# Performance work log

Measured on AMD Instinct MI355X. Metric: run time of the kernel, lower is better.

The kernel has to match this reference:

```python
import jax, jax.numpy as jnp
import numpy as np

N, E, D_IN, HID, D_OUT = 200000, 5000000, 128, 16, 2


def setup_inputs() -> dict:
    key = jax.random.key(0)
    ks = jax.random.split(key, 8)
    x = jax.random.normal(ks[0], (N, D_IN), dtype=jnp.float32)
    edge_index = jax.random.randint(ks[1], (2, E), 0, N, dtype=jnp.int32)
    W1 = jax.random.normal(ks[2], (D_IN, HID), dtype=jnp.float32) / np.sqrt(D_IN)
    b1 = jnp.zeros((HID,), dtype=jnp.float32)
    W3 = jax.random.normal(ks[3], (HID, HID), dtype=jnp.float32) / np.sqrt(HID)
    b3 = jnp.zeros((HID,), dtype=jnp.float32)
    W2 = jax.random.normal(ks[4], (HID, D_OUT), dtype=jnp.float32) / np.sqrt(HID)
    b2 = jnp.zeros((D_OUT,), dtype=jnp.float32)
    return {"x": x, "edge_index": edge_index, "W1": W1, "b1": b1,
            "W3": W3, "b3": b3, "W2": W2, "b2": b2}


def reference(x, edge_index, W1, b1, W3, b3, W2, b2):
    # GCNConv: add self-loops, symmetric normalization, aggregate, linear+bias.
    src, dst = edge_index[0], edge_index[1]
    loops = jnp.arange(N, dtype=src.dtype)
    src_f = jnp.concatenate([src, loops])  # [E+N]
    dst_f = jnp.concatenate([dst, loops])
    deg = jax.ops.segment_sum(jnp.ones_like(src_f, dtype=jnp.float32), dst_f,
                              num_segments=N)
    dis = jnp.where(deg > 0, jax.lax.rsqrt(jnp.maximum(deg, 1.0)), 0.0)
    norm = dis[src_f] * dis[dst_f]  # [E+N]

    def gcn_conv(h, W, b):
        h = h @ W                                   # [N, F_out] small GEMM
        msg = h[src_f] * norm[:, None]              # gather + scale
        agg = jax.ops.segment_sum(msg, dst_f, num_segments=N)  # scatter-add
        return agg + b

    h = jax.nn.relu(gcn_conv(x, W1, b1))    # conv1 (dropout is identity in eval)
    h = jax.nn.relu(gcn_conv(h, W3, b3))    # conv3 loop (conv_number-2 = 1 iter)
    h = gcn_conv(h, W2, b2)                 # conv2
    return jax.nn.log_softmax(h, axis=1)
```

## Files before the change

### kernel.cpp

```cpp
#include <hip/hip_runtime.h>

#define NN 200000
#define NE 5000000
#define DIN 128
#define HID 16
#define DOUT 2
#define BSZ 391
#define NB 512
#define LBITS 9
#define NCH 4
#define SLICE_DIV 50000
#define NK (NB * NCH)
#define NKB 512
#define SKEYS 2048
#define PB 512
#define PT 512
#define ECAP 9216

static_assert((size_t)NB * BSZ >= NN, "bucket coverage");
static_assert((NN - 1) / SLICE_DIV == NCH - 1, "slice count");
static_assert(NE % 8 == 0, "int4-pair edge reads");


__global__ __launch_bounds__(PT) void hist_pass(const int4* __restrict__ dst4,
                                                int* __restrict__ blockHist) {
    __shared__ int h[NKB];
    for (int k = threadIdx.x; k < NKB; k += PT) h[k] = 0;
    __syncthreads();
    const int NI8 = NE / 8;
    for (int j = blockIdx.x * PT + threadIdx.x; j < NI8; j += PB * PT) {
        int4 d0 = dst4[2 * j];
        int4 d1 = dst4[2 * j + 1];
        atomicAdd(&h[d0.x / BSZ], 1);
        atomicAdd(&h[d0.y / BSZ], 1);
        atomicAdd(&h[d0.z / BSZ], 1);
        atomicAdd(&h[d0.w / BSZ], 1);
        atomicAdd(&h[d1.x / BSZ], 1);
        atomicAdd(&h[d1.y / BSZ], 1);
        atomicAdd(&h[d1.z / BSZ], 1);
        atomicAdd(&h[d1.w / BSZ], 1);
    }
    __syncthreads();
    for (int k = threadIdx.x; k < NKB; k += PT)
        blockHist[(size_t)blockIdx.x * NKB + k] = h[k];
}

__global__ __launch_bounds__(256) void tot_pass(const int* __restrict__ blockHist,
                                                int* __restrict__ chunkStart) {
    int k = blockIdx.x * 256 + threadIdx.x;
    if (k >= NKB) return;
    int s = 0;
#pragma unroll 16
    for (int b = 0; b < PB; ++b) s += blockHist[(size_t)b * NKB + k];
    chunkStart[k] = s;
}

__global__ __launch_bounds__(NKB) void scan_keys(int* __restrict__ chunkStart) {
    __shared__ int wsum[8];
    int t = threadIdx.x;
    int lane = t & 63, w = t >> 6;
    int v = chunkStart[t];
    int inc = v;
    for (int off = 1; off < 64; off <<= 1) {
        int nb = __shfl_up(inc, off, 64);
        if (lane >= off) inc += nb;
    }
    if (lane == 63) wsum[w] = inc;
    __syncthreads();
    if (t == 0) {
        int car = 0;
#pragma unroll
        for (int i = 0; i < 8; ++i) { int u = wsum[i]; wsum[i] = car; car += u; }
    }
    __syncthreads();
    chunkStart[t] = inc - v + wsum[w];
    if (t == 0) chunkStart[NKB] = NE;
}

__global__ __launch_bounds__(256) void offsets_pass(int* __restrict__ blockHist,
                                                    const int* __restrict__ chunkStart) {
    int k = blockIdx.x * 256 + threadIdx.x;
    if (k >= NKB) return;
    int r = chunkStart[k];
#pragma unroll 8
    for (int b = 0; b < PB; ++b) {
        size_t idx = (size_t)b * NKB + k;
        int v = blockHist[idx];
        blockHist[idx] = r;
        r += v;
    }
}

__global__ __launch_bounds__(PT) void scatter_pass(const int4* __restrict__ src4,
                                                   const int4* __restrict__ dst4,
                                                   const int* __restrict__ blockHist,
                                                   unsigned* __restrict__ pedge) {
    __shared__ int cur[NKB];
    for (int k = threadIdx.x; k < NKB; k += PT)
        cur[k] = blockHist[(size_t)blockIdx.x * NKB + k];
    __syncthreads();
    const int NI8 = NE / 8;
    for (int j = blockIdx.x * PT + threadIdx.x; j < NI8; j += PB * PT) {
        int4 s0 = src4[2 * j];
        int4 s1 = src4[2 * j + 1];
        int4 d0 = dst4[2 * j];
        int4 d1 = dst4[2 * j + 1];
        int b0 = d0.x / BSZ, b1 = d0.y / BSZ, b2 = d0.z / BSZ, b3 = d0.w / BSZ;
        int b4 = d1.x / BSZ, b5 = d1.y / BSZ, b6 = d1.z / BSZ, b7 = d1.w / BSZ;
        int p0 = atomicAdd(&cur[b0], 1);
        int p1 = atomicAdd(&cur[b1], 1);
        int p2 = atomicAdd(&cur[b2], 1);
        int p3 = atomicAdd(&cur[b3], 1);
        int p4 = atomicAdd(&cur[b4], 1);
        int p5 = atomicAdd(&cur[b5], 1);
        int p6 = atomicAdd(&cur[b6], 1);
        int p7 = atomicAdd(&cur[b7], 1);
        pedge[p0] = ((unsigned)s0.x << LBITS) | (unsigned)(d0.x - b0 * BSZ);
        pedge[p1] = ((unsigned)s0.y << LBITS) | (unsigned)(d0.y - b1 * BSZ);
        pedge[p2] = ((unsigned)s0.z << LBITS) | (unsigned)(d0.z - b2 * BSZ);
        pedge[p3] = ((unsigned)s0.w << LBITS) | (unsigned)(d0.w - b3 * BSZ);
        pedge[p4] = ((unsigned)s1.x << LBITS) | (unsigned)(d1.x - b4 * BSZ);
        pedge[p5] = ((unsigned)s1.y << LBITS) | (unsigned)(d1.y - b5 * BSZ);
        pedge[p6] = ((unsigned)s1.z << LBITS) | (unsigned)(d1.z - b6 * BSZ);
        pedge[p7] = ((unsigned)s1.w << LBITS) | (unsigned)(d1.w - b7 * BSZ);
    }
}


__global__ __launch_bounds__(512) void subsort(const unsigned* __restrict__ pedge,
                                               const int* __restrict__ chunkStart,
                                               int* __restrict__ pedge2,
                                               int* __restrict__ rowStart,
                                               float* __restrict__ dis) {
    __shared__ int h[SKEYS];
    __shared__ unsigned ebuf[ECAP];
    __shared__ int wsum[8];
    int t = threadIdx.x;
    int b = blockIdx.x;
    int lane = t & 63, w = t >> 6;
    int e0 = chunkStart[b], e1 = chunkStart[b + 1];
    int n = e1 - e0;
    for (int k = t; k < SKEYS; k += 512) h[k] = 0;
    __syncthreads();
    for (int i = t; i < n; i += 512) {
        unsigned p = pedge[e0 + i];
        if (i < ECAP) ebuf[i] = p;
        int sv = (int)(p >> LBITS);
        atomicAdd(&h[(sv / SLICE_DIV) * 512 + (p & 511u)], 1);
    }
    __syncthreads();
    if (t < BSZ) {
        int dg = 1;
#pragma unroll
        for (int s = 0; s < NCH; ++s) dg += h[s * 512 + t];
        int node = b * BSZ + t;
        if (node < NN) dis[node] = rsqrtf((float)dg);
    }
    int vals[4];
    int s = 0;
#pragma unroll
    for (int j = 0; j < 4; ++j) { vals[j] = h[t * 4 + j]; s += vals[j]; }
    int inc = s;
    for (int off = 1; off < 64; off <<= 1) {
        int nb = __shfl_up(inc, off, 64);
        if (lane >= off) inc += nb;
    }
    if (lane == 63) wsum[w] = inc;
    __syncthreads();
    if (t == 0) {
        int car = 0;
#pragma unroll
        for (int i = 0; i < 8; ++i) { int u = wsum[i]; wsum[i] = car; car += u; }
    }
    __syncthreads();
    int run = inc - s + wsum[w];
#pragma unroll
    for (int j = 0; j < 4; ++j) {
        int k = t * 4 + j;
        h[k] = run;
        int dl = k & 511, sl = k >> 9;
        if (dl < BSZ)
            rowStart[(size_t)(b * NCH + sl) * BSZ + dl] = e0 + run;
        run += vals[j];
    }
    __syncthreads();
    for (int i = t; i < n; i += 512) {
        unsigned p = (i < ECAP) ? ebuf[i] : pedge[e0 + i];
        int sv = (int)(p >> LBITS);
        int key = (sv / SLICE_DIV) * 512 + (p & 511u);
        int pos = atomicAdd(&h[key], 1);
        pedge2[e0 + pos] = sv;
    }
    if (b == 0 && t == 0) rowStart[(size_t)NK * BSZ] = NE;
}


#define GXT 512
#define GXR 128
__global__ __launch_bounds__(GXT) void gemm_x_w1(const float* __restrict__ x,
                                                 const float* __restrict__ W,
                                                 const float* __restrict__ dis,
                                                 float* __restrict__ out) {
    __shared__ float w[DIN * HID];
    int t = threadIdx.x;
    for (int i = t; i < DIN * HID; i += GXT) w[i] = W[i];
    __syncthreads();
    int row = blockIdx.x * GXR + (t >> 2);
    int c0 = (t & 3) * 4;
    if (row >= NN) return;
    const float4* xr = reinterpret_cast<const float4*>(x + (size_t)row * DIN);
    float ax = 0.f, ay = 0.f, az = 0.f, aw = 0.f;
#pragma unroll
    for (int k4 = 0; k4 < DIN / 4; ++k4) {
        float4 xv = xr[k4];
        float4 w0 = *reinterpret_cast<const float4*>(&w[(4 * k4 + 0) * HID + c0]);
        float4 w1 = *reinterpret_cast<const float4*>(&w[(4 * k4 + 1) * HID + c0]);
        float4 w2 = *reinterpret_cast<const float4*>(&w[(4 * k4 + 2) * HID + c0]);
        float4 w3 = *reinterpret_cast<const float4*>(&w[(4 * k4 + 3) * HID + c0]);
        ax += xv.x * w0.x + xv.y * w1.x + xv.z * w2.x + xv.w * w3.x;
        ay += xv.x * w0.y + xv.y * w1.y + xv.z * w2.y + xv.w * w3.y;
        az += xv.x * w0.z + xv.y * w1.z + xv.z * w2.z + xv.w * w3.z;
        aw += xv.x * w0.w + xv.y * w1.w + xv.z * w2.w + xv.w * w3.w;
    }
    float dd = dis[row];
    *reinterpret_cast<float4*>(&out[(size_t)row * HID + c0]) =
        make_float4(ax * dd, ay * dd, az * dd, aw * dd);
}

__global__ __launch_bounds__(256) void gemm_h_w16(const float* __restrict__ h,
                                                  const float* __restrict__ W,
                                                  const float* __restrict__ dis,
                                                  float* __restrict__ out) {
    __shared__ float w[HID * HID];
    if (threadIdx.x < HID * HID) w[threadIdx.x] = W[threadIdx.x];
    __syncthreads();
    int row = blockIdx.x * 16 + (threadIdx.x >> 4);
    int c = threadIdx.x & 15;
    if (row >= NN) return;
    const float4* hr = reinterpret_cast<const float4*>(h + (size_t)row * HID);
    float acc = 0.f;
#pragma unroll
    for (int k4 = 0; k4 < HID / 4; ++k4) {
        float4 v = hr[k4];
        acc += v.x * w[(4 * k4 + 0) * HID + c] + v.y * w[(4 * k4 + 1) * HID + c]
             + v.z * w[(4 * k4 + 2) * HID + c] + v.w * w[(4 * k4 + 3) * HID + c];
    }
    out[row * HID + c] = acc * dis[row];
}

__global__ __launch_bounds__(256) void gemm_h_w2(const float* __restrict__ h,
                                                 const float* __restrict__ W,
                                                 const float* __restrict__ dis,
                                                 float* __restrict__ out) {
    int t = blockIdx.x * 256 + threadIdx.x;
    int row = t >> 1;
    int c = t & 1;
    if (row >= NN) return;
    const float* hr = h + (size_t)row * HID;
    float acc = 0.f;
#pragma unroll
    for (int k = 0; k < HID; ++k) acc += hr[k] * W[k * DOUT + c];
    out[row * DOUT + c] = acc * dis[row];
}


__device__ __forceinline__ void acc_edges(const int* __restrict__ pedge2,
                                          const float4* __restrict__ xs4,
                                          int e, int e1, int c4, float4& a) {
    for (; e + 3 < e1; e += 4) {
        int s0 = pedge2[e], s1 = pedge2[e + 1];
        int s2 = pedge2[e + 2], s3 = pedge2[e + 3];
        float4 u0 = xs4[(s0 << 2) + c4];
        float4 u1 = xs4[(s1 << 2) + c4];
        float4 u2 = xs4[(s2 << 2) + c4];
        float4 u3 = xs4[(s3 << 2) + c4];
        a.x += (u0.x + u1.x) + (u2.x + u3.x);
        a.y += (u0.y + u1.y) + (u2.y + u3.y);
        a.z += (u0.z + u1.z) + (u2.z + u3.z);
        a.w += (u0.w + u1.w) + (u2.w + u3.w);
    }
    for (; e < e1; ++e) {
        float4 u = xs4[(pedge2[e] << 2) + c4];
        a.x += u.x; a.y += u.y; a.z += u.z; a.w += u.w;
    }
}

__global__ __launch_bounds__(1024, 8) void agg16_all(const int* __restrict__ pedge2,
                                                     const int* __restrict__ rowStart,
                                                     const float* __restrict__ xs,
                                                     const float* __restrict__ dis,
                                                     const float* __restrict__ bias,
                                                     float* __restrict__ buf,
                                                     int relu) {
    int t = threadIdx.x;
    int b = blockIdx.x;
    int base = b * BSZ;
    int c4 = t & 3;
    int q = t >> 2;
    int g0 = (q * BSZ) >> 8;
    int g1 = ((q + 1) * BSZ) >> 8;
    bool two = (g1 - g0) == 2;
    int n0 = base + g0, n1 = base + g0 + 1;
    bool v0 = n0 < NN;
    bool v1 = two && (n1 < NN);
    const float4* xs4 = reinterpret_cast<const float4*>(xs);
    float4* buf4 = reinterpret_cast<float4*>(buf);
    int sA[NCH], sB[NCH], sC[NCH];
#pragma unroll
    for (int r = 0; r < NCH; ++r) {
        const int* rs = rowStart + (size_t)(b * NCH + r) * BSZ + g0;
        sA[r] = v0 ? rs[0] : 0;
        sB[r] = v0 ? rs[1] : 0;
        sC[r] = v1 ? rs[2] : 0;
    }
    float4 a0 = make_float4(0.f, 0.f, 0.f, 0.f);
    float4 a1 = a0;
    if (v0) a0 = xs4[(n0 << 2) + c4];
    if (v1) a1 = xs4[(n1 << 2) + c4];
#pragma unroll
    for (int r = 0; r < NCH; ++r) {
        if (v0) acc_edges(pedge2, xs4, sA[r], sB[r], c4, a0);
        if (v1) acc_edges(pedge2, xs4, sB[r], sC[r], c4, a1);
    }
    float4 bb = reinterpret_cast<const float4*>(bias)[c4];
    if (v0) {
        float dd = dis[n0];
        float4 v = make_float4(dd * a0.x + bb.x, dd * a0.y + bb.y,
                               dd * a0.z + bb.z, dd * a0.w + bb.w);
        if (relu) { v.x = fmaxf(v.x, 0.f); v.y = fmaxf(v.y, 0.f);
                    v.z = fmaxf(v.z, 0.f); v.w = fmaxf(v.w, 0.f); }
        buf4[(n0 << 2) + c4] = v;
    }
    if (v1) {
        float dd = dis[n1];
        float4 v = make_float4(dd * a1.x + bb.x, dd * a1.y + bb.y,
                               dd * a1.z + bb.z, dd * a1.w + bb.w);
        if (relu) { v.x = fmaxf(v.x, 0.f); v.y = fmaxf(v.y, 0.f);
                    v.z = fmaxf(v.z, 0.f); v.w = fmaxf(v.w, 0.f); }
        buf4[(n1 << 2) + c4] = v;
    }
}

__global__ __launch_bounds__(512) void agg2_lsm(const int* __restrict__ pedge2,
                                                const int* __restrict__ rowStart,
                                                const float* __restrict__ xs,
                                                const float* __restrict__ dis,
                                                const float* __restrict__ bias,
                                                float* __restrict__ out) {
    int t = threadIdx.x;
    int b = blockIdx.x;
    if (t >= BSZ) return;
    int node = b * BSZ + t;
    if (node >= NN) return;
    const float2* xs2 = reinterpret_cast<const float2*>(xs);
    float a0 = 0.f, a1 = 0.f;
#pragma unroll
    for (int s = 0; s < NCH; ++s) {
        const int* rs = rowStart + (size_t)(b * NCH + s) * BSZ;
        int e = rs[t], e1 = rs[t + 1];
        for (; e + 3 < e1; e += 4) {
            int s0 = pedge2[e], s1 = pedge2[e + 1];
            int s2 = pedge2[e + 2], s3 = pedge2[e + 3];
            float2 v0 = xs2[s0], v1 = xs2[s1], v2 = xs2[s2], v3 = xs2[s3];
            a0 += (v0.x + v1.x) + (v2.x + v3.x);
            a1 += (v0.y + v1.y) + (v2.y + v3.y);
        }
        for (; e < e1; ++e) {
            float2 v = xs2[pedge2[e]];
            a0 += v.x; a1 += v.y;
        }
    }
    float2 sv = xs2[node];
    float d = dis[node];
    float v0 = (a0 + sv.x) * d + bias[0];
    float v1 = (a1 + sv.y) * d + bias[1];
    float m = fmaxf(v0, v1);
    float lse = m + logf(__expf(v0 - m) + __expf(v1 - m));
    reinterpret_cast<float2*>(out)[node] = make_float2(v0 - lse, v1 - lse);
}


extern "C" void kernel_launch(void* const* d_in, const int* in_sizes, int n_in,
                              void* d_out, int out_size, void* d_ws, size_t ws_size,
                              hipStream_t stream) {
    const float* x = (const float*)d_in[0];
    const int* ei = (const int*)d_in[1];
    const float* W1 = (const float*)d_in[2];
    const float* b1 = (const float*)d_in[3];
    const float* W3 = (const float*)d_in[4];
    const float* b3 = (const float*)d_in[5];
    const float* W2 = (const float*)d_in[6];
    const float* b2 = (const float*)d_in[7];
    float* out = (float*)d_out;

    const int4* src4 = (const int4*)ei;
    const int4* dst4 = (const int4*)(ei + NE);

    int* W = (int*)d_ws;
    unsigned* pedge = (unsigned*)W;
    int* pedge2 = W + NE;
    int* rowStart = W + 2 * (size_t)NE;
    int* blockHist = rowStart + (size_t)NK * BSZ + 4;
    int* chunkStart = blockHist + (size_t)PB * NKB;
    float* dis = (float*)(chunkStart + NKB + 4);
    float* bufB = dis + NN;
    float* bufA = (float*)W;

    const int B = 256;
    auto cdiv = [](long long a, long long b) { return (int)((a + b - 1) / b); };

    hist_pass<<<PB, PT, 0, stream>>>(dst4, blockHist);
    tot_pass<<<cdiv(NKB, 256), 256, 0, stream>>>(blockHist, chunkStart);
    scan_keys<<<1, NKB, 0, stream>>>(chunkStart);
    offsets_pass<<<cdiv(NKB, 256), 256, 0, stream>>>(blockHist, chunkStart);
    scatter_pass<<<PB, PT, 0, stream>>>(src4, dst4, blockHist, pedge);
    subsort<<<NB, 512, 0, stream>>>(pedge, chunkStart, pedge2, rowStart, dis);

    gemm_x_w1<<<cdiv(NN, GXR), GXT, 0, stream>>>(x, W1, dis, bufA);
    agg16_all<<<NB, 1024, 0, stream>>>(pedge2, rowStart, bufA, dis, b1, bufB, 1);

    gemm_h_w16<<<cdiv(NN, 16), B, 0, stream>>>(bufB, W3, dis, bufA);
    agg16_all<<<NB, 1024, 0, stream>>>(pedge2, rowStart, bufA, dis, b3, bufB, 1);

    gemm_h_w2<<<cdiv((long long)NN * DOUT, B), B, 0, stream>>>(bufB, W2, dis, bufA);
    agg2_lsm<<<NB, 512, 0, stream>>>(pedge2, rowStart, bufA, dis, b2, out);
}
```

Before: 276.3 us.

## Fuse next-layer small GEMMs into aggregation epilogues via quad shuffles

Removes the two standalone small-GEMM kernels (h@W3 and h@W2) and folds them into the aggregation kernel's epilogue. After bias and ReLU, each quad of lanes exchanges its 4-column pieces with shuffles and multiplies by the next layer's weights, which are staged in shared memory. For the last layer it reduces to 2 outputs and writes them as a float2. This saves two kernel launches and a full round trip of the 16-wide hidden activations through global memory, at the cost of a little extra epilogue work and a barrier in the aggregation kernel.

```diff
diff --git a/kernel.cpp b/kernel.cpp
--- a/kernel.cpp
+++ b/kernel.cpp
@@ -227,42 +227,6 @@
         make_float4(ax * dd, ay * dd, az * dd, aw * dd);
 }
 
-__global__ __launch_bounds__(256) void gemm_h_w16(const float* __restrict__ h,
-                                                  const float* __restrict__ W,
-                                                  const float* __restrict__ dis,
-                                                  float* __restrict__ out) {
-    __shared__ float w[HID * HID];
-    if (threadIdx.x < HID * HID) w[threadIdx.x] = W[threadIdx.x];
-    __syncthreads();
-    int row = blockIdx.x * 16 + (threadIdx.x >> 4);
-    int c = threadIdx.x & 15;
-    if (row >= NN) return;
-    const float4* hr = reinterpret_cast<const float4*>(h + (size_t)row * HID);
-    float acc = 0.f;
-#pragma unroll
-    for (int k4 = 0; k4 < HID / 4; ++k4) {
-        float4 v = hr[k4];
-        acc += v.x * w[(4 * k4 + 0) * HID + c] + v.y * w[(4 * k4 + 1) * HID + c]
-             + v.z * w[(4 * k4 + 2) * HID + c] + v.w * w[(4 * k4 + 3) * HID + c];
-    }
-    out[row * HID + c] = acc * dis[row];
-}
-
-__global__ __launch_bounds__(256) void gemm_h_w2(const float* __restrict__ h,
-                                                 const float* __restrict__ W,
-                                                 const float* __restrict__ dis,
-                                                 float* __restrict__ out) {
-    int t = blockIdx.x * 256 + threadIdx.x;
-    int row = t >> 1;
-    int c = t & 1;
-    if (row >= NN) return;
-    const float* hr = h + (size_t)row * HID;
-    float acc = 0.f;
-#pragma unroll
-    for (int k = 0; k < HID; ++k) acc += hr[k] * W[k * DOUT + c];
-    out[row * DOUT + c] = acc * dis[row];
-}
-
 
 __device__ __forceinline__ void acc_edges(const int* __restrict__ pedge2,
                                           const float4* __restrict__ xs4,
@@ -285,14 +249,62 @@
     }
 }
 
+__device__ __forceinline__ void epi_store(const float* __restrict__ wl,
+                                          float* __restrict__ buf,
+                                          int node, int c4, const float4& a,
+                                          const float4& bb, float dd, int mode) {
+    float4 h;
+    h.x = fmaxf(dd * a.x + bb.x, 0.f);
+    h.y = fmaxf(dd * a.y + bb.y, 0.f);
+    h.z = fmaxf(dd * a.z + bb.z, 0.f);
+    h.w = fmaxf(dd * a.w + bb.w, 0.f);
+    if (mode == 0) {
+        float4 y = make_float4(0.f, 0.f, 0.f, 0.f);
+        int c0 = c4 * 4;
+#pragma unroll
+        for (int l = 0; l < 4; ++l) {
+            float h0 = __shfl(h.x, l, 4);
+            float h1 = __shfl(h.y, l, 4);
+            float h2 = __shfl(h.z, l, 4);
+            float h3 = __shfl(h.w, l, 4);
+            const float* wr = wl + (4 * l) * HID + c0;
+            float4 w0 = *reinterpret_cast<const float4*>(wr);
+            float4 w1 = *reinterpret_cast<const float4*>(wr + HID);
+            float4 w2 = *reinterpret_cast<const float4*>(wr + 2 * HID);
+            float4 w3 = *reinterpret_cast<const float4*>(wr + 3 * HID);
+            y.x += h0 * w0.x + h1 * w1.x + h2 * w2.x + h3 * w3.x;
+            y.y += h0 * w0.y + h1 * w1.y + h2 * w2.y + h3 * w3.y;
+            y.z += h0 * w0.z + h1 * w1.z + h2 * w2.z + h3 * w3.z;
+            y.w += h0 * w0.w + h1 * w1.w + h2 * w2.w + h3 * w3.w;
+        }
+        reinterpret_cast<float4*>(buf)[(node << 2) + c4] =
+            make_float4(y.x * dd, y.y * dd, y.z * dd, y.w * dd);
+    } else {
+        const float* wr = wl + (4 * c4) * DOUT;
+        float p0 = h.x * wr[0] + h.y * wr[2] + h.z * wr[4] + h.w * wr[6];
+        float p1 = h.x * wr[1] + h.y * wr[3] + h.z * wr[5] + h.w * wr[7];
+        p0 += __shfl_xor(p0, 1, 4);
+        p0 += __shfl_xor(p0, 2, 4);
+        p1 += __shfl_xor(p1, 1, 4);
+        p1 += __shfl_xor(p1, 2, 4);
+        if (c4 == 0)
+            reinterpret_cast<float2*>(buf)[node] = make_float2(p0 * dd, p1 * dd);
+    }
+}
+
 __global__ __launch_bounds__(1024, 8) void agg16_all(const int* __restrict__ pedge2,
                                                      const int* __restrict__ rowStart,
                                                      const float* __restrict__ xs,
                                                      const float* __restrict__ dis,
                                                      const float* __restrict__ bias,
+                                                     const float* __restrict__ Wn,
                                                      float* __restrict__ buf,
-                                                     int relu) {
+                                                     int mode) {
+    __shared__ float wl[HID * HID];
     int t = threadIdx.x;
+    int nw = (mode == 0) ? HID * HID : HID * DOUT;
+    if (t < nw) wl[t] = Wn[t];
+    __syncthreads();
     int b = blockIdx.x;
     int base = b * BSZ;
     int c4 = t & 3;
@@ -304,7 +316,6 @@
     bool v0 = n0 < NN;
     bool v1 = two && (n1 < NN);
     const float4* xs4 = reinterpret_cast<const float4*>(xs);
-    float4* buf4 = reinterpret_cast<float4*>(buf);
     int sA[NCH], sB[NCH], sC[NCH];
 #pragma unroll
     for (int r = 0; r < NCH; ++r) {
@@ -323,22 +334,8 @@
         if (v1) acc_edges(pedge2, xs4, sB[r], sC[r], c4, a1);
     }
     float4 bb = reinterpret_cast<const float4*>(bias)[c4];
-    if (v0) {
-        float dd = dis[n0];
-        float4 v = make_float4(dd * a0.x + bb.x, dd * a0.y + bb.y,
-                               dd * a0.z + bb.z, dd * a0.w + bb.w);
-        if (relu) { v.x = fmaxf(v.x, 0.f); v.y = fmaxf(v.y, 0.f);
-                    v.z = fmaxf(v.z, 0.f); v.w = fmaxf(v.w, 0.f); }
-        buf4[(n0 << 2) + c4] = v;
-    }
-    if (v1) {
-        float dd = dis[n1];
-        float4 v = make_float4(dd * a1.x + bb.x, dd * a1.y + bb.y,
-                               dd * a1.z + bb.z, dd * a1.w + bb.w);
-        if (relu) { v.x = fmaxf(v.x, 0.f); v.y = fmaxf(v.y, 0.f);
-                    v.z = fmaxf(v.z, 0.f); v.w = fmaxf(v.w, 0.f); }
-        buf4[(n1 << 2) + c4] = v;
-    }
+    if (v0) epi_store(wl, buf, n0, c4, a0, bb, dis[n0], mode);
+    if (v1) epi_store(wl, buf, n1, c4, a1, bb, dis[n1], mode);
 }
 
 __global__ __launch_bounds__(512) void agg2_lsm(const int* __restrict__ pedge2,
@@ -406,7 +403,6 @@
     float* bufB = dis + NN;
     float* bufA = (float*)W;
 
-    const int B = 256;
     auto cdiv = [](long long a, long long b) { return (int)((a + b - 1) / b); };
 
     hist_pass<<<PB, PT, 0, stream>>>(dst4, blockHist);
@@ -417,11 +413,9 @@
     subsort<<<NB, 512, 0, stream>>>(pedge, chunkStart, pedge2, rowStart, dis);
 
     gemm_x_w1<<<cdiv(NN, GXR), GXT, 0, stream>>>(x, W1, dis, bufA);
-    agg16_all<<<NB, 1024, 0, stream>>>(pedge2, rowStart, bufA, dis, b1, bufB, 1);
-
-    gemm_h_w16<<<cdiv(NN, 16), B, 0, stream>>>(bufB, W3, dis, bufA);
-    agg16_all<<<NB, 1024, 0, stream>>>(pedge2, rowStart, bufA, dis, b3, bufB, 1);
-
-    gemm_h_w2<<<cdiv((long long)NN * DOUT, B), B, 0, stream>>>(bufB, W2, dis, bufA);
+    agg16_all<<<NB, 1024, 0, stream>>>(pedge2, rowStart, bufA, dis, b1, W3, bufB, 0);
+
+    agg16_all<<<NB, 1024, 0, stream>>>(pedge2, rowStart, bufB, dis, b3, W2, bufA, 1);
+
     agg2_lsm<<<NB, 512, 0, stream>>>(pedge2, rowStart, bufA, dis, b2, out);
 }
```

Measured after the change: 264.4 us. 4.3% less time.
